# Kernel tuning notes

Measured on AMD Instinct MI355X. Metric: run time of the kernel, lower is better.

## Reference

```python
import jax, jax.numpy as jnp
import numpy as np
from itertools import product

NUM_LEVELS = 4
NUM_FEATURES = 4
B, L = 32, 512

def build_kernel(num_features, num_levels):
    # signatory.all_words ordering: words grouped by length 1..num_levels, lexicographic within length
    words = [w for m in range(1, num_levels + 1) for w in product(range(num_features), repeat=m)]
    num_components = num_levels * (num_levels + 1) // 2
    k = np.zeros((num_components, num_features, len(words)), dtype=np.float32)
    for i, word in enumerate(words):
        m = len(word)
        start = m * (m - 1) // 2
        for j, axis in enumerate(word):
            k[start + j, axis, i] = 1.0
    return jnp.asarray(k)

def setup_inputs() -> dict:
    key = jax.random.key(0)
    x = jax.random.normal(key, (B, L, NUM_FEATURES), dtype=jnp.float32)
    return {"x": x, "kernel": build_kernel(NUM_FEATURES, NUM_LEVELS)}

def reference(x, kernel):
    Bn, Ln, F = x.shape
    NF = kernel.shape[-1]  # num_functionals = 340
    # path increments
    seq = x[:, 1:, :] - x[:, :-1, :]                      # (B, L-1, F)
    # lift: (C, B, L-1, NF), C = num_levels*(num_levels+1)/2 = 10
    M = jnp.einsum('blf,cfk->cblk', seq, kernel)
    # level-by-level recursion with independent weights, return_sequences=True
    # then summed over the stacked level axis (stack+sum == running sum of Y terms)
    sig = jnp.cumsum(M[0], axis=1)                        # level 1
    k = 1
    for m in range(1, NUM_LEVELS):
        R = M[k]; k += 1
        for _ in range(m):
            # tf.cumsum(..., exclusive=True) == inclusive cumsum minus self
            R = M[k] * (jnp.cumsum(R, axis=1) - R)
            k += 1
        sig = sig + jnp.cumsum(R, axis=1)
    # prepend zero time step -> (B, L, NF)
    sig = jnp.concatenate([jnp.zeros((Bn, 1, NF), dtype=x.dtype), sig], axis=1)
    # prepend constant-1 functional channel -> (B, L, NF+1)
    return jnp.concatenate([jnp.ones((Bn, Ln, 1), dtype=x.dtype), sig], axis=-1)
```

## Files before the change

kernel.cpp:

```cpp
#include <hip/hip_runtime.h>


#define SIG_B 32
#define SIG_L 512
#define SIG_NSTEP 511
#define SIG_ROW 341
#define SIG_CS 32
#define SIG_C 16
#define SIG_PAD 344

__global__ __launch_bounds__(256) void sigA(const float* __restrict__ x,
                                            float* __restrict__ Lsig) {
    const int bc = blockIdx.x;
    const int b = bc / SIG_C, c = bc % SIG_C;
    const int tid = threadIdx.x;
    const int t0 = c * SIG_CS;
    const int nt = min(SIG_CS, SIG_NSTEP - t0);

    __shared__ float dlds[SIG_CS * 4];
    const float* xb = x + ((size_t)b * SIG_L + t0) * 4;
    if (tid < nt) {
        float4 x0 = *(const float4*)(xb + tid * 4);
        float4 x1 = *(const float4*)(xb + (tid + 1) * 4);
        *(float4*)(dlds + tid * 4) =
            make_float4(x1.x - x0.x, x1.y - x0.y, x1.z - x0.z, x1.w - x0.w);
    }
    __syncthreads();

    const int a = tid >> 6, bb = (tid >> 4) & 3, cc = (tid >> 2) & 3, ee = tid & 3;
    float s1 = 0.f, s2 = 0.f, s3 = 0.f, s4 = 0.f;
    const float* dp = dlds;
    for (int t = 0; t < nt; ++t) {
        const float da = dp[a], db = dp[bb], dc = dp[cc], de = dp[ee];
        dp += 4;
        s4 = fmaf(s3, de, s4);
        s3 = fmaf(s2, dc, s3);
        s2 = fmaf(s1, db, s2);
        s1 += da;
    }
    float* Lr = Lsig + (size_t)bc * SIG_PAD;
    if ((tid & 63) == 0) Lr[1 + a] = s1;
    if ((tid & 15) == 0) Lr[5 + (tid >> 4)] = s2;
    if ((tid & 3) == 0)  Lr[21 + (tid >> 2)] = s3;
    Lr[85 + tid] = s4;
}

__global__ __launch_bounds__(256) void sigB(const float* __restrict__ Lsig,
                                            float* __restrict__ Pws) {
    const int b = blockIdx.x;
    const int tid = threadIdx.x;
    __shared__ float L[SIG_C * SIG_PAD];
    const float* Lb = Lsig + (size_t)b * SIG_C * SIG_PAD;
    for (int i = tid; i < SIG_C * SIG_PAD; i += 256) L[i] = Lb[i];
    __syncthreads();

    const int a = tid >> 6, bb = (tid >> 4) & 3, cc = (tid >> 2) & 3, ee = tid & 3;
    float p1 = 0.f, p2 = 0.f, p3 = 0.f, p4 = 0.f;
    float* Pb = Pws + (size_t)b * SIG_C * SIG_PAD;
    for (int c = 0; c < SIG_C; ++c) {
        float* Pr = Pb + c * SIG_PAD;
        if ((tid & 63) == 0) Pr[1 + a] = p1;
        if ((tid & 15) == 0) Pr[5 + (tid >> 4)] = p2;
        if ((tid & 3) == 0)  Pr[21 + (tid >> 2)] = p3;
        Pr[85 + tid] = p4;
        const float* Lc = L + c * SIG_PAD;
        const float l1a = Lc[1 + a], l1b = Lc[1 + bb], l1c = Lc[1 + cc], l1e = Lc[1 + ee];
        const float l2ab = Lc[5 + 4 * a + bb], l2bc = Lc[5 + 4 * bb + cc],
                    l2ce = Lc[5 + 4 * cc + ee];
        const float l3abc = Lc[21 + 16 * a + 4 * bb + cc],
                    l3bce = Lc[21 + 16 * bb + 4 * cc + ee];
        const float l4 = Lc[85 + tid];
        p4 += p3 * l1e + p2 * l2ce + p1 * l3bce + l4;
        p3 += p2 * l1c + p1 * l2bc + l3abc;
        p2 += p1 * l1b + l2ab;
        p1 += l1a;
    }
}

__global__ __launch_bounds__(256) void sigC(const float* __restrict__ x,
                                            const float* __restrict__ Pws,
                                            float* __restrict__ out) {
    const int bc = blockIdx.x;
    const int b = bc / SIG_C, c = bc % SIG_C;
    const int tid = threadIdx.x;
    const int t0 = c * SIG_CS;
    const int nt = min(SIG_CS, SIG_NSTEP - t0);

    __shared__ float dlds[SIG_CS * 4];
    __shared__ float P[SIG_ROW];
    const float* xb = x + ((size_t)b * SIG_L + t0) * 4;
    if (tid < nt) {
        float4 x0 = *(const float4*)(xb + tid * 4);
        float4 x1 = *(const float4*)(xb + (tid + 1) * 4);
        *(float4*)(dlds + tid * 4) =
            make_float4(x1.x - x0.x, x1.y - x0.y, x1.z - x0.z, x1.w - x0.w);
    }
    const float* Pr = Pws + (size_t)bc * SIG_PAD;
    for (int i = tid; i < SIG_ROW; i += 256) P[i] = Pr[i];
    __syncthreads();

    const int a = tid >> 6, bb = (tid >> 4) & 3, cc = (tid >> 2) & 3, ee = tid & 3;
    const float p1 = P[1 + a];
    const float p2 = P[5 + 4 * a + bb];
    const float p3 = P[21 + 16 * a + 4 * bb + cc];
    const float p4 = P[85 + tid];

    float s1 = 0.f, s2 = 0.f, s3 = 0.f, s4 = 0.f;
    float x1_ = 0.f, x2_ = 0.f, x3_ = 0.f;
    float v1 = 0.f, v2 = 0.f;
    float u1 = 0.f;

    float* row = out + ((size_t)b * SIG_L + (t0 + 1)) * SIG_ROW;

    if (c == 0) {
        float* r0 = out + (size_t)b * SIG_L * SIG_ROW;
        if (tid == 0)        r0[0] = 1.0f;
        if ((tid & 63) == 0) r0[1 + a] = 0.f;
        if ((tid & 15) == 0) r0[5 + (tid >> 4)] = 0.f;
        if ((tid & 3) == 0)  r0[21 + (tid >> 2)] = 0.f;
        r0[85 + tid] = 0.f;
    }

    const float* dp = dlds;
    for (int t = 0; t < nt; ++t) {
        const float da = dp[a], db = dp[bb], dc = dp[cc], de = dp[ee];
        dp += 4;
        s4 = fmaf(s3, de, s4); s3 = fmaf(s2, dc, s3); s2 = fmaf(s1, db, s2); s1 += da;
        x3_ = fmaf(x2_, de, x3_); x2_ = fmaf(x1_, dc, x2_); x1_ += db;
        v2 = fmaf(v1, de, v2); v1 += dc;
        u1 += de;

        if (tid == 0)        row[0] = 1.0f;
        if ((tid & 63) == 0) row[1 + a] = p1 + s1;
        if ((tid & 15) == 0) row[5 + (tid >> 4)] = p2 + p1 * x1_ + s2;
        if ((tid & 3) == 0)  row[21 + (tid >> 2)] = p3 + p2 * v1 + p1 * x2_ + s3;
        row[85 + tid] = p4 + p3 * u1 + p2 * v2 + p1 * x3_ + s4;
        row += SIG_ROW;
    }
}

extern "C" void kernel_launch(void* const* d_in, const int* in_sizes, int n_in,
                              void* d_out, int out_size, void* d_ws, size_t ws_size,
                              hipStream_t stream) {
    const float* x = (const float*)d_in[0];
    float* out = (float*)d_out;
    float* Lsig = (float*)d_ws;
    float* Pws  = Lsig + (size_t)SIG_B * SIG_C * SIG_PAD;

    sigA<<<SIG_B * SIG_C, 256, 0, stream>>>(x, Lsig);
    sigB<<<SIG_B, 256, 0, stream>>>(Lsig, Pws);
    sigC<<<SIG_B * SIG_C, 256, 0, stream>>>(x, Pws, out);
}
```

Measured before the change: 24.87 us.

## Fuse chunk-prefix combine into output kernel and use nontemporal stores

Removes the separate serial prefix kernel (sigB). Each output block now recomputes the signature prefix from the local chunk signatures of all earlier chunks, using Chen's identity, before it writes its rows. This saves one launch and a global round trip through the P workspace. In exchange each block loads up to 15 chunk rows and repeats the combine work, so later blocks do more work. Output writes become nontemporal stores to reduce cache pollution.

```diff
diff --git a/kernel.cpp b/kernel.cpp
--- a/kernel.cpp
+++ b/kernel.cpp
@@ -45,25 +45,38 @@
     Lr[85 + tid] = s4;
 }
 
-__global__ __launch_bounds__(256) void sigB(const float* __restrict__ Lsig,
-                                            float* __restrict__ Pws) {
-    const int b = blockIdx.x;
+__global__ __launch_bounds__(256) void sigC(const float* __restrict__ x,
+                                            const float* __restrict__ Lsig,
+                                            float* __restrict__ out) {
+    const int bc = blockIdx.x;
+    const int b = bc / SIG_C, c = bc % SIG_C;
     const int tid = threadIdx.x;
+    const int t0 = c * SIG_CS;
+    const int nt = min(SIG_CS, SIG_NSTEP - t0);
+
+    __shared__ float dlds[SIG_CS * 4];
     __shared__ float L[SIG_C * SIG_PAD];
-    const float* Lb = Lsig + (size_t)b * SIG_C * SIG_PAD;
-    for (int i = tid; i < SIG_C * SIG_PAD; i += 256) L[i] = Lb[i];
+
+    const float* xb = x + ((size_t)b * SIG_L + t0) * 4;
+    if (tid < nt) {
+        float4 x0 = *(const float4*)(xb + tid * 4);
+        float4 x1 = *(const float4*)(xb + (tid + 1) * 4);
+        *(float4*)(dlds + tid * 4) =
+            make_float4(x1.x - x0.x, x1.y - x0.y, x1.z - x0.z, x1.w - x0.w);
+    }
+    {
+        const float4* Lb4 = (const float4*)(Lsig + (size_t)b * SIG_C * SIG_PAD);
+        float4* L4 = (float4*)L;
+        const int n4 = c * (SIG_PAD / 4);
+        for (int i = tid; i < n4; i += 256) L4[i] = Lb4[i];
+    }
     __syncthreads();
 
     const int a = tid >> 6, bb = (tid >> 4) & 3, cc = (tid >> 2) & 3, ee = tid & 3;
+
     float p1 = 0.f, p2 = 0.f, p3 = 0.f, p4 = 0.f;
-    float* Pb = Pws + (size_t)b * SIG_C * SIG_PAD;
-    for (int c = 0; c < SIG_C; ++c) {
-        float* Pr = Pb + c * SIG_PAD;
-        if ((tid & 63) == 0) Pr[1 + a] = p1;
-        if ((tid & 15) == 0) Pr[5 + (tid >> 4)] = p2;
-        if ((tid & 3) == 0)  Pr[21 + (tid >> 2)] = p3;
-        Pr[85 + tid] = p4;
-        const float* Lc = L + c * SIG_PAD;
+    for (int j = 0; j < c; ++j) {
+        const float* Lc = L + j * SIG_PAD;
         const float l1a = Lc[1 + a], l1b = Lc[1 + bb], l1c = Lc[1 + cc], l1e = Lc[1 + ee];
         const float l2ab = Lc[5 + 4 * a + bb], l2bc = Lc[5 + 4 * bb + cc],
                     l2ce = Lc[5 + 4 * cc + ee];
@@ -75,35 +88,6 @@
         p2 += p1 * l1b + l2ab;
         p1 += l1a;
     }
-}
-
-__global__ __launch_bounds__(256) void sigC(const float* __restrict__ x,
-                                            const float* __restrict__ Pws,
-                                            float* __restrict__ out) {
-    const int bc = blockIdx.x;
-    const int b = bc / SIG_C, c = bc % SIG_C;
-    const int tid = threadIdx.x;
-    const int t0 = c * SIG_CS;
-    const int nt = min(SIG_CS, SIG_NSTEP - t0);
-
-    __shared__ float dlds[SIG_CS * 4];
-    __shared__ float P[SIG_ROW];
-    const float* xb = x + ((size_t)b * SIG_L + t0) * 4;
-    if (tid < nt) {
-        float4 x0 = *(const float4*)(xb + tid * 4);
-        float4 x1 = *(const float4*)(xb + (tid + 1) * 4);
-        *(float4*)(dlds + tid * 4) =
-            make_float4(x1.x - x0.x, x1.y - x0.y, x1.z - x0.z, x1.w - x0.w);
-    }
-    const float* Pr = Pws + (size_t)bc * SIG_PAD;
-    for (int i = tid; i < SIG_ROW; i += 256) P[i] = Pr[i];
-    __syncthreads();
-
-    const int a = tid >> 6, bb = (tid >> 4) & 3, cc = (tid >> 2) & 3, ee = tid & 3;
-    const float p1 = P[1 + a];
-    const float p2 = P[5 + 4 * a + bb];
-    const float p3 = P[21 + 16 * a + 4 * bb + cc];
-    const float p4 = P[85 + tid];
 
     float s1 = 0.f, s2 = 0.f, s3 = 0.f, s4 = 0.f;
     float x1_ = 0.f, x2_ = 0.f, x3_ = 0.f;
@@ -114,11 +98,11 @@
 
     if (c == 0) {
         float* r0 = out + (size_t)b * SIG_L * SIG_ROW;
-        if (tid == 0)        r0[0] = 1.0f;
-        if ((tid & 63) == 0) r0[1 + a] = 0.f;
-        if ((tid & 15) == 0) r0[5 + (tid >> 4)] = 0.f;
-        if ((tid & 3) == 0)  r0[21 + (tid >> 2)] = 0.f;
-        r0[85 + tid] = 0.f;
+        if (tid == 0)        __builtin_nontemporal_store(1.0f, r0 + 0);
+        if ((tid & 63) == 0) __builtin_nontemporal_store(0.f, r0 + 1 + a);
+        if ((tid & 15) == 0) __builtin_nontemporal_store(0.f, r0 + 5 + (tid >> 4));
+        if ((tid & 3) == 0)  __builtin_nontemporal_store(0.f, r0 + 21 + (tid >> 2));
+        __builtin_nontemporal_store(0.f, r0 + 85 + tid);
     }
 
     const float* dp = dlds;
@@ -130,11 +114,14 @@
         v2 = fmaf(v1, de, v2); v1 += dc;
         u1 += de;
 
-        if (tid == 0)        row[0] = 1.0f;
-        if ((tid & 63) == 0) row[1 + a] = p1 + s1;
-        if ((tid & 15) == 0) row[5 + (tid >> 4)] = p2 + p1 * x1_ + s2;
-        if ((tid & 3) == 0)  row[21 + (tid >> 2)] = p3 + p2 * v1 + p1 * x2_ + s3;
-        row[85 + tid] = p4 + p3 * u1 + p2 * v2 + p1 * x3_ + s4;
+        if (tid == 0)        __builtin_nontemporal_store(1.0f, row + 0);
+        if ((tid & 63) == 0) __builtin_nontemporal_store(p1 + s1, row + 1 + a);
+        if ((tid & 15) == 0) __builtin_nontemporal_store(p2 + p1 * x1_ + s2,
+                                                         row + 5 + (tid >> 4));
+        if ((tid & 3) == 0)  __builtin_nontemporal_store(p3 + p2 * v1 + p1 * x2_ + s3,
+                                                         row + 21 + (tid >> 2));
+        __builtin_nontemporal_store(p4 + p3 * u1 + p2 * v2 + p1 * x3_ + s4,
+                                    row + 85 + tid);
         row += SIG_ROW;
     }
 }
@@ -145,9 +132,7 @@
     const float* x = (const float*)d_in[0];
     float* out = (float*)d_out;
     float* Lsig = (float*)d_ws;
-    float* Pws  = Lsig + (size_t)SIG_B * SIG_C * SIG_PAD;
 
     sigA<<<SIG_B * SIG_C, 256, 0, stream>>>(x, Lsig);
-    sigB<<<SIG_B, 256, 0, stream>>>(Lsig, Pws);
-    sigC<<<SIG_B * SIG_C, 256, 0, stream>>>(x, Pws, out);
+    sigC<<<SIG_B * SIG_C, 256, 0, stream>>>(x, Lsig, out);
 }
```

Result: faster. 22.20 us (-10.7%).
